# Optimization experiments

Hardware: AMD Instinct MI355X
Metric: run time of the kernel (lower is better)

Reference implementation:

```python
import jax, jax.numpy as jnp
import numpy as np

B = 4096          # batch_size per view
D = 256           # projection feature dim
TEMP_F = 0.5      # temperature_f


def setup_inputs() -> dict:
    key = jax.random.key(0)
    k1, k2 = jax.random.split(key)
    return {
        "h_i": jax.random.normal(k1, (B, D), dtype=jnp.float32),
        "h_j": jax.random.normal(k2, (B, D), dtype=jnp.float32),
    }


def reference(h_i, h_j):
    # NT-Xent contrastive loss (forward_feature).
    batch = h_i.shape[0]
    N = 2 * batch
    h = jnp.concatenate([h_i, h_j], axis=0)                 # [N, D]
    sim = (h @ h.T) / TEMP_F                                # [N, N]

    # positives: sim(i, i+batch) and sim(i+batch, i)
    sim_i_j = jnp.diagonal(sim, offset=batch)               # [batch]
    sim_j_i = jnp.diagonal(sim, offset=-batch)              # [batch]
    pos = jnp.concatenate([sim_i_j, sim_j_i], axis=0)       # [N]

    # Torch builds logits = [pos_i, negatives_i] per row where negatives are
    # sim[i, :] with the diagonal AND the positive-pair entry removed, then
    # takes CE with label 0. Since the removed positive-pair entry equals
    # pos_i itself, logsumexp(logits_i) == logsumexp(sim[i, :] with only the
    # diagonal masked). So: loss_i = logsumexp(sim_masked[i]) - pos_i.
    neg_inf = jnp.finfo(sim.dtype).min
    eye = jnp.eye(N, dtype=bool)
    sim_masked = jnp.where(eye, neg_inf, sim)               # mask self-similarity
    lse = jax.nn.logsumexp(sim_masked, axis=1)              # [N]

    # CrossEntropyLoss(reduction='sum') / N  == mean over rows
    loss = jnp.mean(lse - pos)
    return loss
```

## Files before the change

### kernel.cpp

```cpp
#include <hip/hip_runtime.h>
#include <hip/hip_bf16.h>
#include <stdint.h>

#define BATCH 4096
#define N_TOT 8192
#define D_DIM 256
#define SHIFT 150.0f
#define SQRT2 1.41421356237309515f

typedef float f32x4 __attribute__((ext_vector_type(4)));

__device__ __forceinline__ void gl_lds16(const void* g, void* l) {
  __builtin_amdgcn_global_load_lds(
      (const __attribute__((address_space(1))) void*)(uintptr_t)g,
      (__attribute__((address_space(3))) void*)(uint32_t)(uintptr_t)l,
      16, 0, 0);
}

__global__ void k_prep(const float* __restrict__ hi, const float* __restrict__ hj,
                       uint8_t* __restrict__ hb8, float* __restrict__ Zrow,
                       float* __restrict__ posPartial) {
  const int wave = threadIdx.x >> 6, lane = threadIdx.x & 63;
  const int r = blockIdx.x * 4 + wave;
  const size_t off = (size_t)r * D_DIM + lane * 4;
  float4 a = *(const float4*)(hi + off);
  float4 b = *(const float4*)(hj + off);

  int wa = __builtin_amdgcn_cvt_pk_fp8_f32(a.x * SQRT2, a.y * SQRT2, 0, false);
  wa = __builtin_amdgcn_cvt_pk_fp8_f32(a.z * SQRT2, a.w * SQRT2, wa, true);
  int wb = __builtin_amdgcn_cvt_pk_fp8_f32(b.x * SQRT2, b.y * SQRT2, 0, false);
  wb = __builtin_amdgcn_cvt_pk_fp8_f32(b.z * SQRT2, b.w * SQRT2, wb, true);
  *(int*)(hb8 + (size_t)r * D_DIM + lane * 4) = wa;
  *(int*)(hb8 + (size_t)(BATCH + r) * D_DIM + lane * 4) = wb;

  float d = a.x * b.x + a.y * b.y + a.z * b.z + a.w * b.w;
#pragma unroll
  for (int o = 32; o >= 1; o >>= 1) d += __shfl_xor(d, o);
  __shared__ float ps[4];
  if (lane == 0) ps[wave] = d;
  if (threadIdx.x < 8) Zrow[blockIdx.x * 8 + threadIdx.x] = 0.f;
  __syncthreads();
  if (threadIdx.x == 0) posPartial[blockIdx.x] = ps[0] + ps[1] + ps[2] + ps[3];
}

__global__ __launch_bounds__(256, 2) void k_gemm(const uint8_t* __restrict__ hb8,
                                                 float* __restrict__ Zrow) {
  const int t = blockIdx.x;
  int bj = (int)((sqrtf(8.0f * (float)t + 1.0f) - 1.0f) * 0.5f);
  while ((bj + 1) * (bj + 2) / 2 <= t) ++bj;
  while (bj * (bj + 1) / 2 > t) --bj;
  const int bi = t - bj * (bj + 1) / 2;
  const int rBase = bi * 128;
  const int cBase = bj * 128;
  const bool diag = (bi == bj);

  __shared__ __align__(16) uint8_t As[128 * 256];
  __shared__ __align__(16) uint8_t Bs[128 * 256];
  const int lane = threadIdx.x & 63;
  const int wave = threadIdx.x >> 6;

  {
    const int half = wave & 1;
    const int gbase = (wave < 2 ? rBase : cBase) + half * 64;
    uint8_t* lbase = (wave < 2 ? As : Bs) + half * 64 * 256;
    const int rowOff = lane >> 4, c16 = lane & 15;
#pragma unroll
    for (int i = 0; i < 16; ++i) {
      const int r = i * 4 + rowOff;
      const uint8_t* src = hb8 + (size_t)(gbase + r) * 256 + ((c16 ^ (r & 15)) * 16);
      gl_lds16(src, lbase + i * 1024 + lane * 16);
    }
  }
  __syncthreads();

  const int wm = wave >> 1, wn = wave & 1;
  const int quad = lane >> 4, l16 = lane & 15;

  f32x4 acc[4][4];
#pragma unroll
  for (int i = 0; i < 4; ++i)
#pragma unroll
    for (int j = 0; j < 4; ++j) acc[i][j] = (f32x4){0.f, 0.f, 0.f, 0.f};

#pragma unroll
  for (int ks = 0; ks < 8; ++ks) {
    const int j = ks * 4 + quad;
    const int off = (((j >> 1) ^ l16) * 16) + (j & 1) * 8;
    long a[4], b[4];
#pragma unroll
    for (int mt = 0; mt < 4; ++mt)
      a[mt] = *(const long*)(As + (wm * 64 + mt * 16 + l16) * 256 + off);
#pragma unroll
    for (int nt = 0; nt < 4; ++nt)
      b[nt] = *(const long*)(Bs + (wn * 64 + nt * 16 + l16) * 256 + off);
#pragma unroll
    for (int mt = 0; mt < 4; ++mt)
#pragma unroll
      for (int nt = 0; nt < 4; ++nt)
        acc[mt][nt] = __builtin_amdgcn_mfma_f32_16x16x32_fp8_fp8(a[mt], b[nt],
                                                                 acc[mt][nt], 0, 0, 0);
  }

  const int rW = rBase + wm * 64 + quad * 4;
  const int cW = cBase + wn * 64 + l16;
  float colAcc[4] = {0.f, 0.f, 0.f, 0.f};
#pragma unroll
  for (int mt = 0; mt < 4; ++mt) {
#pragma unroll
    for (int rg = 0; rg < 4; ++rg) {
      const int rr = rW + mt * 16 + rg;
      float s = 0.f;
#pragma unroll
      for (int nt = 0; nt < 4; ++nt) {
        float e = __expf(acc[mt][nt][rg] - SHIFT);
        if (diag && (rr == cW + nt * 16)) e = 0.f;
        s += e;
        colAcc[nt] += e;
      }
      s += __shfl_xor(s, 1);
      s += __shfl_xor(s, 2);
      s += __shfl_xor(s, 4);
      s += __shfl_xor(s, 8);
      if (l16 == 0) atomicAdd(&Zrow[rr], s);
    }
  }
  if (!diag) {
#pragma unroll
    for (int nt = 0; nt < 4; ++nt) {
      float c = colAcc[nt];
      c += __shfl_xor(c, 16);
      c += __shfl_xor(c, 32);
      if (lane < 16) atomicAdd(&Zrow[cW + nt * 16], c);
    }
  }
}

__global__ void k_finish(const float* __restrict__ Zrow,
                         const float* __restrict__ posPartial,
                         float* __restrict__ out) {
  const int t = threadIdx.x;
  float4 z0 = *(const float4*)(Zrow + t * 8);
  float4 z1 = *(const float4*)(Zrow + t * 8 + 4);
  float sl = __logf(z0.x) + __logf(z0.y) + __logf(z0.z) + __logf(z0.w) +
             __logf(z1.x) + __logf(z1.y) + __logf(z1.z) + __logf(z1.w);
  float sp = posPartial[t];
#pragma unroll
  for (int o = 32; o >= 1; o >>= 1) {
    sl += __shfl_xor(sl, o);
    sp += __shfl_xor(sp, o);
  }
  __shared__ float pl[16], pp[16];
  const int wave = t >> 6, lane = t & 63;
  if (lane == 0) { pl[wave] = sl; pp[wave] = sp; }
  __syncthreads();
  if (t == 0) {
    float L = 0.f, P = 0.f;
    for (int i = 0; i < 16; ++i) { L += pl[i]; P += pp[i]; }
    out[0] = L / (float)N_TOT + SHIFT - P / 2048.0f;
  }
}

extern "C" void kernel_launch(void* const* d_in, const int* in_sizes, int n_in,
                              void* d_out, int out_size, void* d_ws, size_t ws_size,
                              hipStream_t stream) {
  const float* hi = (const float*)d_in[0];
  const float* hj = (const float*)d_in[1];
  float* out = (float*)d_out;

  uint8_t* hb8 = (uint8_t*)d_ws;
  float* Zrow = (float*)((char*)d_ws + (size_t)N_TOT * D_DIM);
  float* posPartial = Zrow + N_TOT;

  k_prep<<<1024, 256, 0, stream>>>(hi, hj, hb8, Zrow, posPartial);
  k_gemm<<<2080, 256, 0, stream>>>(hb8, Zrow);
  k_finish<<<1, 1024, 0, stream>>>(Zrow, posPartial, out);
}
```

Baseline: 101.0 us.

## Permute fp8 K layout for 16-byte LDS reads; replace atomics with partial-sum slices

The prep kernel now writes the fp8 rows in a permuted K order, so each lane fetches 16 bytes per LDS read and issues two MFMAs per load instead of one 8-byte load per MFMA. The row and column exp sums are no longer atomically added into one Zrow array. Each tile writes plain stores into per-tile-column slices of a 128 x N partial buffer. A new reduce kernel then sums the slices and takes the log. This removes atomic contention and halves the LDS read instruction count, at the cost of an extra kernel launch and about 4 MB of partial-sum traffic.

```diff
diff --git a/kernel.cpp b/kernel.cpp
--- a/kernel.cpp
+++ b/kernel.cpp
@@ -9,6 +9,7 @@
 #define SQRT2 1.41421356237309515f
 
 typedef float f32x4 __attribute__((ext_vector_type(4)));
+typedef long lx2 __attribute__((ext_vector_type(2)));
 
 __device__ __forceinline__ void gl_lds16(const void* g, void* l) {
   __builtin_amdgcn_global_load_lds(
@@ -18,8 +19,7 @@
 }
 
 __global__ void k_prep(const float* __restrict__ hi, const float* __restrict__ hj,
-                       uint8_t* __restrict__ hb8, float* __restrict__ Zrow,
-                       float* __restrict__ posPartial) {
+                       uint8_t* __restrict__ hb8T, float* __restrict__ posPartial) {
   const int wave = threadIdx.x >> 6, lane = threadIdx.x & 63;
   const int r = blockIdx.x * 4 + wave;
   const size_t off = (size_t)r * D_DIM + lane * 4;
@@ -30,21 +30,23 @@
   wa = __builtin_amdgcn_cvt_pk_fp8_f32(a.z * SQRT2, a.w * SQRT2, wa, true);
   int wb = __builtin_amdgcn_cvt_pk_fp8_f32(b.x * SQRT2, b.y * SQRT2, 0, false);
   wb = __builtin_amdgcn_cvt_pk_fp8_f32(b.z * SQRT2, b.w * SQRT2, wb, true);
-  *(int*)(hb8 + (size_t)r * D_DIM + lane * 4) = wa;
-  *(int*)(hb8 + (size_t)(BATCH + r) * D_DIM + lane * 4) = wb;
+
+  const int toff = ((lane >> 1) & 3) * 64 + (lane >> 4) * 16 +
+                   ((lane >> 3) & 1) * 8 + (lane & 1) * 4;
+  *(int*)(hb8T + (size_t)r * 256 + toff) = wa;
+  *(int*)(hb8T + (size_t)(BATCH + r) * 256 + toff) = wb;
 
   float d = a.x * b.x + a.y * b.y + a.z * b.z + a.w * b.w;
 #pragma unroll
   for (int o = 32; o >= 1; o >>= 1) d += __shfl_xor(d, o);
   __shared__ float ps[4];
   if (lane == 0) ps[wave] = d;
-  if (threadIdx.x < 8) Zrow[blockIdx.x * 8 + threadIdx.x] = 0.f;
   __syncthreads();
   if (threadIdx.x == 0) posPartial[blockIdx.x] = ps[0] + ps[1] + ps[2] + ps[3];
 }
 
-__global__ __launch_bounds__(256, 2) void k_gemm(const uint8_t* __restrict__ hb8,
-                                                 float* __restrict__ Zrow) {
+__global__ __launch_bounds__(256, 2) void k_gemm(const uint8_t* __restrict__ hb8T,
+                                                 float* __restrict__ Zpart) {
   const int t = blockIdx.x;
   int bj = (int)((sqrtf(8.0f * (float)t + 1.0f) - 1.0f) * 0.5f);
   while ((bj + 1) * (bj + 2) / 2 <= t) ++bj;
@@ -67,7 +69,7 @@
 #pragma unroll
     for (int i = 0; i < 16; ++i) {
       const int r = i * 4 + rowOff;
-      const uint8_t* src = hb8 + (size_t)(gbase + r) * 256 + ((c16 ^ (r & 15)) * 16);
+      const uint8_t* src = hb8T + (size_t)(gbase + r) * 256 + ((c16 ^ (r & 15)) * 16);
       gl_lds16(src, lbase + i * 1024 + lane * 16);
     }
   }
@@ -83,26 +85,30 @@
     for (int j = 0; j < 4; ++j) acc[i][j] = (f32x4){0.f, 0.f, 0.f, 0.f};
 
 #pragma unroll
-  for (int ks = 0; ks < 8; ++ks) {
-    const int j = ks * 4 + quad;
-    const int off = (((j >> 1) ^ l16) * 16) + (j & 1) * 8;
-    long a[4], b[4];
+  for (int ks2 = 0; ks2 < 4; ++ks2) {
+    const int slot = ((quad * 4 + ks2) ^ l16) * 16;
+    lx2 a[4], b[4];
 #pragma unroll
     for (int mt = 0; mt < 4; ++mt)
-      a[mt] = *(const long*)(As + (wm * 64 + mt * 16 + l16) * 256 + off);
+      a[mt] = *(const lx2*)(As + (wm * 64 + mt * 16 + l16) * 256 + slot);
 #pragma unroll
     for (int nt = 0; nt < 4; ++nt)
-      b[nt] = *(const long*)(Bs + (wn * 64 + nt * 16 + l16) * 256 + off);
+      b[nt] = *(const lx2*)(Bs + (wn * 64 + nt * 16 + l16) * 256 + slot);
 #pragma unroll
     for (int mt = 0; mt < 4; ++mt)
 #pragma unroll
-      for (int nt = 0; nt < 4; ++nt)
-        acc[mt][nt] = __builtin_amdgcn_mfma_f32_16x16x32_fp8_fp8(a[mt], b[nt],
+      for (int nt = 0; nt < 4; ++nt) {
+        acc[mt][nt] = __builtin_amdgcn_mfma_f32_16x16x32_fp8_fp8(a[mt].x, b[nt].x,
                                                                  acc[mt][nt], 0, 0, 0);
+        acc[mt][nt] = __builtin_amdgcn_mfma_f32_16x16x32_fp8_fp8(a[mt].y, b[nt].y,
+                                                                 acc[mt][nt], 0, 0, 0);
+      }
   }
 
   const int rW = rBase + wm * 64 + quad * 4;
   const int cW = cBase + wn * 64 + l16;
+  float* rowSlice = Zpart + (size_t)(2 * bj + wn) * N_TOT;
+  float* colSlice = Zpart + (size_t)(2 * bi + wm) * N_TOT;
   float colAcc[4] = {0.f, 0.f, 0.f, 0.f};
 #pragma unroll
   for (int mt = 0; mt < 4; ++mt) {
@@ -121,7 +127,7 @@
       s += __shfl_xor(s, 2);
       s += __shfl_xor(s, 4);
       s += __shfl_xor(s, 8);
-      if (l16 == 0) atomicAdd(&Zrow[rr], s);
+      if (l16 == 0) rowSlice[rr] = s;
     }
   }
   if (!diag) {
@@ -130,19 +136,32 @@
       float c = colAcc[nt];
       c += __shfl_xor(c, 16);
       c += __shfl_xor(c, 32);
-      if (lane < 16) atomicAdd(&Zrow[cW + nt * 16], c);
+      if (lane < 16) colSlice[cW + nt * 16] = c;
     }
   }
 }
 
-__global__ void k_finish(const float* __restrict__ Zrow,
+__global__ void k_reduce(const float* __restrict__ Zpart,
+                         float* __restrict__ lsePartial) {
+  const int r = blockIdx.x * 256 + threadIdx.x;
+  float z = 0.f;
+#pragma unroll
+  for (int s = 0; s < 128; ++s) z += Zpart[(size_t)s * N_TOT + r];
+  float v = __logf(z);
+#pragma unroll
+  for (int o = 32; o >= 1; o >>= 1) v += __shfl_xor(v, o);
+  __shared__ float ps[4];
+  const int wave = threadIdx.x >> 6, lane = threadIdx.x & 63;
+  if (lane == 0) ps[wave] = v;
+  __syncthreads();
+  if (threadIdx.x == 0) lsePartial[blockIdx.x] = ps[0] + ps[1] + ps[2] + ps[3];
+}
+
+__global__ void k_finish(const float* __restrict__ lsePartial,
                          const float* __restrict__ posPartial,
                          float* __restrict__ out) {
   const int t = threadIdx.x;
-  float4 z0 = *(const float4*)(Zrow + t * 8);
-  float4 z1 = *(const float4*)(Zrow + t * 8 + 4);
-  float sl = __logf(z0.x) + __logf(z0.y) + __logf(z0.z) + __logf(z0.w) +
-             __logf(z1.x) + __logf(z1.y) + __logf(z1.z) + __logf(z1.w);
+  float sl = (t < 32) ? lsePartial[t] : 0.f;
   float sp = posPartial[t];
 #pragma unroll
   for (int o = 32; o >= 1; o >>= 1) {
@@ -167,11 +186,13 @@
   const float* hj = (const float*)d_in[1];
   float* out = (float*)d_out;
 
-  uint8_t* hb8 = (uint8_t*)d_ws;
-  float* Zrow = (float*)((char*)d_ws + (size_t)N_TOT * D_DIM);
-  float* posPartial = Zrow + N_TOT;
+  uint8_t* hb8T = (uint8_t*)d_ws;
+  float* Zpart = (float*)((char*)d_ws + (size_t)N_TOT * D_DIM);
+  float* posPartial = Zpart + (size_t)128 * N_TOT;
+  float* lsePartial = posPartial + 1024;
 
-  k_prep<<<1024, 256, 0, stream>>>(hi, hj, hb8, Zrow, posPartial);
-  k_gemm<<<2080, 256, 0, stream>>>(hb8, Zrow);
-  k_finish<<<1, 1024, 0, stream>>>(Zrow, posPartial, out);
+  k_prep<<<1024, 256, 0, stream>>>(hi, hj, hb8T, posPartial);
+  k_gemm<<<2080, 256, 0, stream>>>(hb8T, Zpart);
+  k_reduce<<<32, 256, 0, stream>>>(Zpart, lsePartial);
+  k_finish<<<1, 1024, 0, stream>>>(lsePartial, posPartial, out);
 }
```

Measured after the change: 126.0 us. 24.7% more time.

## Make GEMM blocks persistent over column tiles, reusing A tile and prefetching B

Applied to the files above, without the earlier changes.

The triangular GEMM now launches 512 blocks. Each block keeps its 128-row A tile in LDS and walks column tiles bj = bi+s, bi+s+8, and so on. The next B tile is loaded asynchronously during the exp/atomic epilogue. The prep kernel writes fp8 rows in a permuted k-order so each lane can read 16 bytes per LDS load and feed two MFMAs. This is meant to cut repeated A loads and expose load/compute overlap, but it adds load imbalance across blocks (some bi+s combinations exit early) and fewer blocks overall.

```diff
diff --git a/kernel.cpp b/kernel.cpp
--- a/kernel.cpp
+++ b/kernel.cpp
@@ -9,6 +9,7 @@
 #define SQRT2 1.41421356237309515f
 
 typedef float f32x4 __attribute__((ext_vector_type(4)));
+typedef long lx2 __attribute__((ext_vector_type(2)));
 
 __device__ __forceinline__ void gl_lds16(const void* g, void* l) {
   __builtin_amdgcn_global_load_lds(
@@ -18,7 +19,7 @@
 }
 
 __global__ void k_prep(const float* __restrict__ hi, const float* __restrict__ hj,
-                       uint8_t* __restrict__ hb8, float* __restrict__ Zrow,
+                       uint8_t* __restrict__ hb8T, float* __restrict__ Zrow,
                        float* __restrict__ posPartial) {
   const int wave = threadIdx.x >> 6, lane = threadIdx.x & 63;
   const int r = blockIdx.x * 4 + wave;
@@ -30,8 +31,11 @@
   wa = __builtin_amdgcn_cvt_pk_fp8_f32(a.z * SQRT2, a.w * SQRT2, wa, true);
   int wb = __builtin_amdgcn_cvt_pk_fp8_f32(b.x * SQRT2, b.y * SQRT2, 0, false);
   wb = __builtin_amdgcn_cvt_pk_fp8_f32(b.z * SQRT2, b.w * SQRT2, wb, true);
-  *(int*)(hb8 + (size_t)r * D_DIM + lane * 4) = wa;
-  *(int*)(hb8 + (size_t)(BATCH + r) * D_DIM + lane * 4) = wb;
+
+  const int toff = ((lane >> 1) & 3) * 64 + (lane >> 4) * 16 +
+                   ((lane >> 3) & 1) * 8 + (lane & 1) * 4;
+  *(int*)(hb8T + (size_t)r * 256 + toff) = wa;
+  *(int*)(hb8T + (size_t)(BATCH + r) * 256 + toff) = wb;
 
   float d = a.x * b.x + a.y * b.y + a.z * b.z + a.w * b.w;
 #pragma unroll
@@ -43,94 +47,116 @@
   if (threadIdx.x == 0) posPartial[blockIdx.x] = ps[0] + ps[1] + ps[2] + ps[3];
 }
 
-__global__ __launch_bounds__(256, 2) void k_gemm(const uint8_t* __restrict__ hb8,
+__global__ __launch_bounds__(256, 2) void k_gemm(const uint8_t* __restrict__ hb8T,
                                                  float* __restrict__ Zrow) {
-  const int t = blockIdx.x;
-  int bj = (int)((sqrtf(8.0f * (float)t + 1.0f) - 1.0f) * 0.5f);
-  while ((bj + 1) * (bj + 2) / 2 <= t) ++bj;
-  while (bj * (bj + 1) / 2 > t) --bj;
-  const int bi = t - bj * (bj + 1) / 2;
-  const int rBase = bi * 128;
-  const int cBase = bj * 128;
-  const bool diag = (bi == bj);
+  const int bi = blockIdx.x & 63;
+  const int s = blockIdx.x >> 6;
+  if (bi + s >= 64) return;
 
   __shared__ __align__(16) uint8_t As[128 * 256];
   __shared__ __align__(16) uint8_t Bs[128 * 256];
   const int lane = threadIdx.x & 63;
   const int wave = threadIdx.x >> 6;
-
+  const int rowOff = lane >> 4, c16 = lane & 15;
+  const int rBase = bi * 128;
+
+#pragma unroll
+  for (int i = 0; i < 8; ++i) {
+    const int idx = wave * 8 + i;
+    const int r = idx * 4 + rowOff;
+    gl_lds16(hb8T + (size_t)(rBase + r) * 256 + ((c16 ^ (r & 15)) * 16),
+             As + idx * 1024 + lane * 16);
+  }
   {
-    const int half = wave & 1;
-    const int gbase = (wave < 2 ? rBase : cBase) + half * 64;
-    uint8_t* lbase = (wave < 2 ? As : Bs) + half * 64 * 256;
-    const int rowOff = lane >> 4, c16 = lane & 15;
-#pragma unroll
-    for (int i = 0; i < 16; ++i) {
-      const int r = i * 4 + rowOff;
-      const uint8_t* src = hb8 + (size_t)(gbase + r) * 256 + ((c16 ^ (r & 15)) * 16);
-      gl_lds16(src, lbase + i * 1024 + lane * 16);
-    }
-  }
-  __syncthreads();
+    const int cBase0 = (bi + s) * 128;
+#pragma unroll
+    for (int i = 0; i < 8; ++i) {
+      const int idx = wave * 8 + i;
+      const int r = idx * 4 + rowOff;
+      gl_lds16(hb8T + (size_t)(cBase0 + r) * 256 + ((c16 ^ (r & 15)) * 16),
+               Bs + idx * 1024 + lane * 16);
+    }
+  }
 
   const int wm = wave >> 1, wn = wave & 1;
   const int quad = lane >> 4, l16 = lane & 15;
 
-  f32x4 acc[4][4];
-#pragma unroll
-  for (int i = 0; i < 4; ++i)
-#pragma unroll
-    for (int j = 0; j < 4; ++j) acc[i][j] = (f32x4){0.f, 0.f, 0.f, 0.f};
-
-#pragma unroll
-  for (int ks = 0; ks < 8; ++ks) {
-    const int j = ks * 4 + quad;
-    const int off = (((j >> 1) ^ l16) * 16) + (j & 1) * 8;
-    long a[4], b[4];
-#pragma unroll
-    for (int mt = 0; mt < 4; ++mt)
-      a[mt] = *(const long*)(As + (wm * 64 + mt * 16 + l16) * 256 + off);
-#pragma unroll
-    for (int nt = 0; nt < 4; ++nt)
-      b[nt] = *(const long*)(Bs + (wn * 64 + nt * 16 + l16) * 256 + off);
-#pragma unroll
-    for (int mt = 0; mt < 4; ++mt)
+  for (int bj = bi + s; bj < 64; bj += 8) {
+    __syncthreads();
+
+    f32x4 acc[4][4];
+#pragma unroll
+    for (int i = 0; i < 4; ++i)
+#pragma unroll
+      for (int j = 0; j < 4; ++j) acc[i][j] = (f32x4){0.f, 0.f, 0.f, 0.f};
+
+#pragma unroll
+    for (int ks2 = 0; ks2 < 4; ++ks2) {
+      const int slot = ((quad * 4 + ks2) ^ l16) * 16;
+      lx2 a[4], b[4];
+#pragma unroll
+      for (int mt = 0; mt < 4; ++mt)
+        a[mt] = *(const lx2*)(As + (wm * 64 + mt * 16 + l16) * 256 + slot);
 #pragma unroll
       for (int nt = 0; nt < 4; ++nt)
-        acc[mt][nt] = __builtin_amdgcn_mfma_f32_16x16x32_fp8_fp8(a[mt], b[nt],
-                                                                 acc[mt][nt], 0, 0, 0);
-  }
-
-  const int rW = rBase + wm * 64 + quad * 4;
-  const int cW = cBase + wn * 64 + l16;
-  float colAcc[4] = {0.f, 0.f, 0.f, 0.f};
-#pragma unroll
-  for (int mt = 0; mt < 4; ++mt) {
-#pragma unroll
-    for (int rg = 0; rg < 4; ++rg) {
-      const int rr = rW + mt * 16 + rg;
-      float s = 0.f;
+        b[nt] = *(const lx2*)(Bs + (wn * 64 + nt * 16 + l16) * 256 + slot);
+#pragma unroll
+      for (int mt = 0; mt < 4; ++mt)
+#pragma unroll
+        for (int nt = 0; nt < 4; ++nt) {
+          acc[mt][nt] = __builtin_amdgcn_mfma_f32_16x16x32_fp8_fp8(
+              a[mt].x, b[nt].x, acc[mt][nt], 0, 0, 0);
+          acc[mt][nt] = __builtin_amdgcn_mfma_f32_16x16x32_fp8_fp8(
+              a[mt].y, b[nt].y, acc[mt][nt], 0, 0, 0);
+        }
+    }
+
+    __syncthreads();
+
+    if (bj + 8 < 64) {
+      const int cBaseN = (bj + 8) * 128;
+#pragma unroll
+      for (int i = 0; i < 8; ++i) {
+        const int idx = wave * 8 + i;
+        const int r = idx * 4 + rowOff;
+        gl_lds16(hb8T + (size_t)(cBaseN + r) * 256 + ((c16 ^ (r & 15)) * 16),
+                 Bs + idx * 1024 + lane * 16);
+      }
+    }
+
+    const bool diag = (bj == bi);
+    const int cBase = bj * 128;
+    const int rW = rBase + wm * 64 + quad * 4;
+    const int cW = cBase + wn * 64 + l16;
+    float colAcc[4] = {0.f, 0.f, 0.f, 0.f};
+#pragma unroll
+    for (int mt = 0; mt < 4; ++mt) {
+#pragma unroll
+      for (int rg = 0; rg < 4; ++rg) {
+        const int rr = rW + mt * 16 + rg;
+        float sv = 0.f;
+#pragma unroll
+        for (int nt = 0; nt < 4; ++nt) {
+          float e = __expf(acc[mt][nt][rg] - SHIFT);
+          if (diag && (rr == cW + nt * 16)) e = 0.f;
+          sv += e;
+          colAcc[nt] += e;
+        }
+        sv += __shfl_xor(sv, 1);
+        sv += __shfl_xor(sv, 2);
+        sv += __shfl_xor(sv, 4);
+        sv += __shfl_xor(sv, 8);
+        if (l16 == 0) atomicAdd(&Zrow[rr], sv);
+      }
+    }
+    if (!diag) {
 #pragma unroll
       for (int nt = 0; nt < 4; ++nt) {
-        float e = __expf(acc[mt][nt][rg] - SHIFT);
-        if (diag && (rr == cW + nt * 16)) e = 0.f;
-        s += e;
-        colAcc[nt] += e;
+        float c = colAcc[nt];
+        c += __shfl_xor(c, 16);
+        c += __shfl_xor(c, 32);
+        if (lane < 16) atomicAdd(&Zrow[cW + nt * 16], c);
       }
-      s += __shfl_xor(s, 1);
-      s += __shfl_xor(s, 2);
-      s += __shfl_xor(s, 4);
-      s += __shfl_xor(s, 8);
-      if (l16 == 0) atomicAdd(&Zrow[rr], s);
-    }
-  }
-  if (!diag) {
-#pragma unroll
-    for (int nt = 0; nt < 4; ++nt) {
-      float c = colAcc[nt];
-      c += __shfl_xor(c, 16);
-      c += __shfl_xor(c, 32);
-      if (lane < 16) atomicAdd(&Zrow[cW + nt * 16], c);
     }
   }
 }
@@ -167,11 +193,11 @@
   const float* hj = (const float*)d_in[1];
   float* out = (float*)d_out;
 
-  uint8_t* hb8 = (uint8_t*)d_ws;
+  uint8_t* hb8T = (uint8_t*)d_ws;
   float* Zrow = (float*)((char*)d_ws + (size_t)N_TOT * D_DIM);
   float* posPartial = Zrow + N_TOT;
 
-  k_prep<<<1024, 256, 0, stream>>>(hi, hj, hb8, Zrow, posPartial);
-  k_gemm<<<2080, 256, 0, stream>>>(hb8, Zrow);
+  k_prep<<<1024, 256, 0, stream>>>(hi, hj, hb8T, Zrow, posPartial);
+  k_gemm<<<512, 256, 0, stream>>>(hb8T, Zrow);
   k_finish<<<1, 1024, 0, stream>>>(Zrow, posPartial, out);
 }
```

Result: slower. 108.4 us (+7.4%).
